# Optimization experiments

Hardware: AMD Instinct MI355X
Metric: run time of the kernel (lower is better)

Reference implementation:

```python
import jax, jax.numpy as jnp
import numpy as np

B, CIN, COUT, H, W = 16, 64, 64, 256, 256
MX, MY = 64, 64  # retained spectral modes (NxW, NyW)
NY_R = W // 2 + 1  # rfft length of last dim


def _dequant(q, scale, min_val):
    # matches torch: (q.float() + 127) * scale + min_val, q in [-127, 128]
    return (q.astype(jnp.float32) + 127.0) * scale + min_val


def setup_inputs() -> dict:
    key = jax.random.key(0)
    k0, k1, k2, k3 = jax.random.split(key, 4)
    x = jax.random.normal(k0, (B, CIN, H, W), dtype=jnp.float32)
    q_real = jax.random.randint(k1, (CIN, COUT, MX, MY), -127, 129, dtype=jnp.int32)
    q_imag = jax.random.randint(k2, (CIN, COUT, MX, MY), -127, 129, dtype=jnp.int32)
    q_bias = jax.random.randint(k3, (COUT,), -127, 129, dtype=jnp.int32)
    return {
        "x": x,
        "q_real": q_real,
        "q_imag": q_imag,
        "q_bias": q_bias,
        "scale_real": jnp.float32(2e-3),
        "min_real": jnp.float32(-0.25),
        "scale_imag": jnp.float32(2e-3),
        "min_imag": jnp.float32(-0.25),
        "b_scale": jnp.float32(1e-4),
        "b_min": jnp.float32(-0.0128),
    }


def reference(x, q_real, q_imag, q_bias, scale_real, min_real, scale_imag, min_imag, b_scale, b_min):
    # 1) rFFT over the last two (spatial) dims, norm='backward' (torch default)
    x_fft = jnp.fft.rfftn(x, axes=(-2, -1), norm="backward")  # [B, Cin, H, NY_R] complex

    # 2) inline dequantize the complex spectral weight
    w_real = _dequant(q_real, scale_real, min_real)
    w_imag = _dequant(q_imag, scale_imag, min_imag)
    Wc = jax.lax.complex(w_real, w_imag)  # [Cin, Cout, MX, MY]

    # 3) center slices as in the torch forward
    cx, nx = H // 2, MX // 2
    sx = slice(cx - nx, cx + (MX - nx))
    cy, ny = NY_R // 2, MY // 2
    sy = slice(cy - ny, cy + (MY - ny))

    # fused channel multiply-accumulate (replaces the nested python loop)
    out_slice = jnp.einsum("bixy,ioxy->boxy", x_fft[:, :, sx, sy], Wc)

    out_fft = jnp.zeros((B, COUT, H, NY_R), dtype=x_fft.dtype)
    out_fft = out_fft.at[:, :, sx, sy].set(out_slice)

    # 4) inverse rFFT back to spatial domain
    x_out = jnp.fft.irfftn(out_fft, s=(H, W), axes=(-2, -1), norm="backward")

    # 5) dequantized bias, broadcast over (1, Cout, 1, 1)
    bias = _dequant(q_bias, b_scale, b_min)
    return x_out + bias[None, :, None, None]
```

## Files before the change

kernel.cpp:

```cpp
#include <hip/hip_runtime.h>


#define HW    256
#define NCIN  64
#define NCOUT 64
#define NB    16
#define R0    96
#define C0    32

typedef __bf16 bf16x2 __attribute__((ext_vector_type(2)));
typedef __bf16 bf16x8 __attribute__((ext_vector_type(8)));
typedef float  f32x4  __attribute__((ext_vector_type(4)));

__device__ __forceinline__ unsigned short f2bf(float f) {
    __bf16 h = (__bf16)f;
    return __builtin_bit_cast(unsigned short, h);
}
__device__ __forceinline__ unsigned pk2(float a, float b) {
    bf16x2 v;
    v.x = (__bf16)a;
    v.y = (__bf16)b;
    return __builtin_bit_cast(unsigned, v);
}
__device__ __forceinline__ bf16x8 ld_frag_g(const unsigned short* p) {
    return __builtin_bit_cast(bf16x8, *(const uint4*)p);
}
__device__ __forceinline__ void gload_lds16(const unsigned short* g, unsigned short* l) {
    __builtin_amdgcn_global_load_lds(
        (const __attribute__((address_space(1))) unsigned int*)g,
        (__attribute__((address_space(3))) unsigned int*)l, 16, 0, 0);
}

__global__ void build_tables2(unsigned short* __restrict__ A1tab,
                              unsigned short* __restrict__ B2T) {
    int idx = blockIdx.x * 256 + threadIdx.x;
    int h = idx >> 7;
    int k = idx & 127;
    int kk = k & 63;
    const float TPO = 0.0245436926061702596754f;
    float s, c;
    int m1 = (((R0 + kk) * h) & 255);
    sincosf((float)m1 * TPO, &s, &c);
    A1tab[idx] = f2bf(k < 64 ? c : s);
    int m2 = (((C0 + kk) * h) & 255);
    sincosf((float)m2 * TPO, &s, &c);
    B2T[idx] = f2bf(k < 64 ? c : -s);
}

__global__ void build_fwd_tables(unsigned short* __restrict__ B1fT,
                                 unsigned short* __restrict__ A2f) {
    int idx = blockIdx.x * 256 + threadIdx.x;
    const float TPO = 0.0245436926061702596754f;
    float s, c;
    if (idx < 32768) {
        int cc = idx >> 8, w = idx & 255;
        int m = (((C0 + (cc & 63)) * w) & 255);
        sincosf((float)m * TPO, &s, &c);
        int sidx = (cc << 8) | (w ^ ((cc & 7) << 3));
        B1fT[sidx] = f2bf(cc < 64 ? c : -s);
    } else {
        int j = idx - 32768;
        int mr = j >> 9, k = j & 511;
        int m = (((R0 + (mr & 63)) * (k & 255)) & 255);
        sincosf((float)m * TPO, &s, &c);
        float v = (mr < 64) ? ((k < 256) ? c : s)
                            : ((k < 256) ? -s : c);
        A2f[j] = f2bf(v);
    }
}

__global__ __launch_bounds__(256, 2) void fwd_mfma(
        const float*          __restrict__ x,
        const unsigned short* __restrict__ B1fT,
        const unsigned short* __restrict__ A2f,
        float*                __restrict__ Xout) {
    __shared__ __align__(16) unsigned short smem[32768];
    int bi = blockIdx.x;
    const float* xim = x + (size_t)bi * 65536;
    int t = threadIdx.x, lane = t & 63, wv = t >> 6;
    int g = lane >> 4, lr = lane & 15;

    #pragma unroll
    for (int i = 0; i < 16; ++i)
        gload_lds16(B1fT + i * 2048 + t * 8, &smem[i * 2048 + wv * 512]);

    const float* xrow[4];
    #pragma unroll
    for (int mf = 0; mf < 4; ++mf)
        xrow[mf] = xim + (wv * 64 + mf * 16 + lr) * 256 + g * 8;
    float4 xv[2][4][2];
    #pragma unroll
    for (int mf = 0; mf < 4; ++mf) {
        xv[0][mf][0] = *(const float4*)(xrow[mf]);
        xv[0][mf][1] = *(const float4*)(xrow[mf] + 4);
    }
    __syncthreads();

    f32x4 acc[4][8];
    #pragma unroll
    for (int mf = 0; mf < 4; ++mf)
        #pragma unroll
        for (int nf = 0; nf < 8; ++nf) acc[mf][nf] = (f32x4)0.0f;

    #pragma unroll
    for (int ks = 0; ks < 8; ++ks) {
        const int cur = ks & 1;
        if (ks < 7) {
            #pragma unroll
            for (int mf = 0; mf < 4; ++mf) {
                xv[cur ^ 1][mf][0] = *(const float4*)(xrow[mf] + (ks + 1) * 32);
                xv[cur ^ 1][mf][1] = *(const float4*)(xrow[mf] + (ks + 1) * 32 + 4);
            }
        }
        int k0 = ks * 32 + g * 8;
        bf16x8 b[8];
        #pragma unroll
        for (int nf = 0; nf < 8; ++nf) {
            int n = nf * 16 + lr;
            b[nf] = __builtin_bit_cast(bf16x8,
                      *(const uint4*)&smem[n * 256 + (k0 ^ ((n & 7) << 3))]);
        }
        bf16x8 a[4];
        #pragma unroll
        for (int mf = 0; mf < 4; ++mf) {
            uint4 pk;
            pk.x = pk2(xv[cur][mf][0].x, xv[cur][mf][0].y);
            pk.y = pk2(xv[cur][mf][0].z, xv[cur][mf][0].w);
            pk.z = pk2(xv[cur][mf][1].x, xv[cur][mf][1].y);
            pk.w = pk2(xv[cur][mf][1].z, xv[cur][mf][1].w);
            a[mf] = __builtin_bit_cast(bf16x8, pk);
        }
        #pragma unroll
        for (int mf = 0; mf < 4; ++mf)
            #pragma unroll
            for (int nf = 0; nf < 8; ++nf)
                acc[mf][nf] = __builtin_amdgcn_mfma_f32_16x16x32_bf16(
                                  a[mf], b[nf], acc[mf][nf], 0, 0, 0);
    }
    __syncthreads();

    #pragma unroll
    for (int mf = 0; mf < 4; ++mf)
        #pragma unroll
        for (int nf = 0; nf < 8; ++nf) {
            int cl  = nf * 16 + lr;
            int col = cl & 63;
            int h0  = wv * 64 + mf * 16 + g * 4;
            int kk0 = (cl < 64) ? h0 : (256 + h0);
            uint2 pk;
            pk.x = pk2(acc[mf][nf][0], acc[mf][nf][1]);
            pk.y = pk2(acc[mf][nf][2], acc[mf][nf][3]);
            *(uint2*)&smem[col * 512 + (kk0 ^ ((col & 7) << 3))] = pk;
        }
    __syncthreads();

    f32x4 acc2[2][4];
    #pragma unroll
    for (int mf = 0; mf < 2; ++mf)
        #pragma unroll
        for (int nf = 0; nf < 4; ++nf) acc2[mf][nf] = (f32x4)0.0f;
    #pragma unroll
    for (int ks = 0; ks < 16; ++ks) {
        int k0 = ks * 32 + g * 8;
        bf16x8 a2[2], b2[4];
        #pragma unroll
        for (int mf = 0; mf < 2; ++mf) {
            int m = wv * 32 + mf * 16 + lr;
            a2[mf] = ld_frag_g(A2f + m * 512 + k0);
        }
        #pragma unroll
        for (int nf = 0; nf < 4; ++nf) {
            int c = nf * 16 + lr;
            b2[nf] = __builtin_bit_cast(bf16x8,
                       *(const uint4*)&smem[c * 512 + (k0 ^ ((c & 7) << 3))]);
        }
        #pragma unroll
        for (int mf = 0; mf < 2; ++mf)
            #pragma unroll
            for (int nf = 0; nf < 4; ++nf)
                acc2[mf][nf] = __builtin_amdgcn_mfma_f32_16x16x32_bf16(
                                   a2[mf], b2[nf], acc2[mf][nf], 0, 0, 0);
    }
    float* Xp = Xout + (size_t)bi * 8192;
    #pragma unroll
    for (int mf = 0; mf < 2; ++mf)
        #pragma unroll
        for (int nf = 0; nf < 4; ++nf)
            #pragma unroll
            for (int rg = 0; rg < 4; ++rg) {
                int m = wv * 32 + mf * 16 + g * 4 + rg;
                int c = nf * 16 + lr;
                Xp[(m >> 6) * 4096 + (m & 63) * 64 + c] = acc2[mf][nf][rg];
            }
}

__global__ __launch_bounds__(256) void mix_kernel(
        const float* __restrict__ X,
        const int*   __restrict__ q_real,
        const int*   __restrict__ q_imag,
        const float* __restrict__ s_r, const float* __restrict__ m_r,
        const float* __restrict__ s_i, const float* __restrict__ m_i,
        float2*      __restrict__ Y) {
    int rr = blockIdx.x;
    int ot = blockIdx.y;
    int t  = threadIdx.x;
    int cp = t & 31;
    int oq = t >> 5;
    int o  = ot * 8 + oq;
    int c0 = cp * 2;
    float sr = *s_r, mr = *m_r, si = *s_i, mi = *m_i;

    __shared__ float xr_sh[2][16][72];
    __shared__ float xi_sh[2][16][72];

    int sb  = t >> 4;
    int scq = t & 15;
    const float* xbase = X + (size_t)sb * 64 * 8192 + rr * 64 + scq * 4;

    const int* qrp = q_real + (size_t)o * 4096 + rr * 64 + c0;
    const int* qip = q_imag + (size_t)o * 4096 + rr * 64 + c0;

    float Yr0[16], Yi0[16], Yr1[16], Yi1[16];
    #pragma unroll
    for (int b = 0; b < 16; ++b) { Yr0[b] = 0.f; Yi0[b] = 0.f; Yr1[b] = 0.f; Yi1[b] = 0.f; }

    int2 wqr[2], wqi[2];
    wqr[0] = *(const int2*)(qrp);
    wqi[0] = *(const int2*)(qip);
    wqr[1] = *(const int2*)(qrp + 262144);
    wqi[1] = *(const int2*)(qip + 262144);
    {
        float4 gr = *(const float4*)(xbase);
        float4 gi = *(const float4*)(xbase + 4096);
        *(float4*)&xr_sh[0][sb][scq * 4] = gr;
        *(float4*)&xi_sh[0][sb][scq * 4] = gi;
    }
    __syncthreads();

    #pragma unroll 2
    for (int i = 0; i < 64; ++i) {
        const int cur = i & 1;
        float4 gr, gi;
        if (i < 63) {
            gr = *(const float4*)(xbase + (size_t)(i + 1) * 8192);
            gi = *(const float4*)(xbase + (size_t)(i + 1) * 8192 + 4096);
        }
        float wr0 = (float)(wqr[cur].x + 127) * sr + mr;
        float wr1 = (float)(wqr[cur].y + 127) * sr + mr;
        float wi0 = (float)(wqi[cur].x + 127) * si + mi;
        float wi1 = (float)(wqi[cur].y + 127) * si + mi;
        if (i < 62) {
            wqr[cur] = *(const int2*)(qrp + (size_t)(i + 2) * 262144);
            wqi[cur] = *(const int2*)(qip + (size_t)(i + 2) * 262144);
        }
        #pragma unroll
        for (int b = 0; b < 16; ++b) {
            float2 xr = *(const float2*)&xr_sh[cur][b][c0];
            float2 xi = *(const float2*)&xi_sh[cur][b][c0];
            Yr0[b] += xr.x * wr0 - xi.x * wi0;
            Yi0[b] += xr.x * wi0 + xi.x * wr0;
            Yr1[b] += xr.y * wr1 - xi.y * wi1;
            Yi1[b] += xr.y * wi1 + xi.y * wr1;
        }
        if (i < 63) {
            *(float4*)&xr_sh[cur ^ 1][sb][scq * 4] = gr;
            *(float4*)&xi_sh[cur ^ 1][sb][scq * 4] = gi;
            __syncthreads();
        }
    }

    #pragma unroll
    for (int b = 0; b < 16; ++b) {
        float4 v = make_float4(Yr0[b], Yi0[b], Yr1[b], Yi1[b]);
        *(float4*)&Y[(size_t)b * 262144 + (size_t)o * 4096 + rr * 64 + c0] = v;
    }
}

__global__ __launch_bounds__(256, 2) void inv_mfma(
        const float2*         __restrict__ Y,
        const unsigned short* __restrict__ A1tab,
        const unsigned short* __restrict__ B2T,
        const int*            __restrict__ q_bias,
        const float* __restrict__ b_s, const float* __restrict__ b_m,
        float*                __restrict__ out) {
    __shared__ __align__(16) unsigned short smem[32768];
    int bo   = blockIdx.x;
    int t    = threadIdx.x;
    int lane = t & 63;
    int wv   = t >> 6;
    int g    = lane >> 4;
    int lr   = lane & 15;
    float bias = ((float)q_bias[bo & 63] + 127.0f) * (*b_s) + (*b_m);

    const float2* Yp = Y + (size_t)bo * 4096;
    for (int l = t; l < 4096; l += 256) {
        int r = l >> 6, c = l & 63;
        float2 y = Yp[l];
        unsigned short yr  = f2bf(y.x);
        unsigned short yi  = f2bf(y.y);
        unsigned short nyi = f2bf(-y.y);
        int sw = (c & 7) << 3;
        smem[c * 128        + ((r)      ^ sw)] = yr;
        smem[c * 128        + ((64 + r) ^ sw)] = nyi;
        smem[(64 + c) * 128 + ((r)      ^ sw)] = yi;
        smem[(64 + c) * 128 + ((64 + r) ^ sw)] = yr;
    }
    __syncthreads();

    f32x4 acc[4][8];
    #pragma unroll
    for (int mf = 0; mf < 4; ++mf)
        #pragma unroll
        for (int nf = 0; nf < 8; ++nf) acc[mf][nf] = (f32x4)0.0f;

    #pragma unroll
    for (int ks = 0; ks < 4; ++ks) {
        int k0 = ks * 32 + g * 8;
        bf16x8 a[4], b[8];
        #pragma unroll
        for (int mf = 0; mf < 4; ++mf) {
            int h = wv * 64 + mf * 16 + lr;
            a[mf] = ld_frag_g(A1tab + h * 128 + k0);
        }
        #pragma unroll
        for (int nf = 0; nf < 8; ++nf) {
            int n = nf * 16 + lr;
            b[nf] = ld_frag_g(&smem[n * 128 + (k0 ^ ((n & 7) << 3))]);
        }
        #pragma unroll
        for (int mf = 0; mf < 4; ++mf)
            #pragma unroll
            for (int nf = 0; nf < 8; ++nf)
                acc[mf][nf] = __builtin_amdgcn_mfma_f32_16x16x32_bf16(
                                  a[mf], b[nf], acc[mf][nf], 0, 0, 0);
    }
    __syncthreads();

    #pragma unroll
    for (int mf = 0; mf < 4; ++mf)
        #pragma unroll
        for (int nf = 0; nf < 8; ++nf)
            #pragma unroll
            for (int rg = 0; rg < 4; ++rg) {
                int h = wv * 64 + mf * 16 + g * 4 + rg;
                int k = nf * 16 + lr;
                smem[h * 128 + (k ^ ((h & 7) << 3))] = f2bf(acc[mf][nf][rg]);
            }
    __syncthreads();

    const float scale = 2.0f / 65536.0f;
    float* outp = out + (size_t)bo * 65536;
    #pragma unroll
    for (int nh = 0; nh < 2; ++nh) {
        f32x4 acc2[4][8];
        #pragma unroll
        for (int mf = 0; mf < 4; ++mf)
            #pragma unroll
            for (int nf = 0; nf < 8; ++nf) acc2[mf][nf] = (f32x4)0.0f;

        #pragma unroll
        for (int ks = 0; ks < 4; ++ks) {
            int k0 = ks * 32 + g * 8;
            bf16x8 a[4], b[8];
            #pragma unroll
            for (int mf = 0; mf < 4; ++mf) {
                int h = wv * 64 + mf * 16 + lr;
                a[mf] = ld_frag_g(&smem[h * 128 + (k0 ^ ((h & 7) << 3))]);
            }
            #pragma unroll
            for (int nf = 0; nf < 8; ++nf) {
                int w = nh * 128 + nf * 16 + lr;
                b[nf] = ld_frag_g(B2T + w * 128 + k0);
            }
            #pragma unroll
            for (int mf = 0; mf < 4; ++mf)
                #pragma unroll
                for (int nf = 0; nf < 8; ++nf)
                    acc2[mf][nf] = __builtin_amdgcn_mfma_f32_16x16x32_bf16(
                                       a[mf], b[nf], acc2[mf][nf], 0, 0, 0);
        }
        #pragma unroll
        for (int mf = 0; mf < 4; ++mf)
            #pragma unroll
            for (int rg = 0; rg < 4; ++rg) {
                int h = wv * 64 + mf * 16 + g * 4 + rg;
                float* row = outp + h * 256 + nh * 128 + lr;
                #pragma unroll
                for (int nf = 0; nf < 8; ++nf)
                    row[nf * 16] = acc2[mf][nf][rg] * scale + bias;
            }
    }
}

extern "C" void kernel_launch(void* const* d_in, const int* in_sizes, int n_in,
                              void* d_out, int out_size, void* d_ws, size_t ws_size,
                              hipStream_t stream) {
    const float* x          = (const float*)d_in[0];
    const int*   q_real     = (const int*)  d_in[1];
    const int*   q_imag     = (const int*)  d_in[2];
    const int*   q_bias     = (const int*)  d_in[3];
    const float* scale_real = (const float*)d_in[4];
    const float* min_real   = (const float*)d_in[5];
    const float* scale_imag = (const float*)d_in[6];
    const float* min_imag   = (const float*)d_in[7];
    const float* b_scale    = (const float*)d_in[8];
    const float* b_min      = (const float*)d_in[9];
    float* out = (float*)d_out;

    float* ws = (float*)d_ws;
    unsigned short* A1tab = (unsigned short*)(ws);
    unsigned short* B2T   = (unsigned short*)(ws + 16384);
    unsigned short* B1fT  = (unsigned short*)(ws + 32768);
    unsigned short* A2f   = (unsigned short*)(ws + 49152);
    float*          Xws   = (float*) (ws + 81920);
    float2*         Yws   = (float2*)(ws + 81920 + 8388608);

    build_tables2<<<128, 256, 0, stream>>>(A1tab, B2T);
    build_fwd_tables<<<384, 256, 0, stream>>>(B1fT, A2f);
    fwd_mfma<<<NB * NCIN, 256, 0, stream>>>(x, B1fT, A2f, Xws);
    mix_kernel<<<dim3(64, 8), 256, 0, stream>>>(Xws, q_real, q_imag,
                                                scale_real, min_real,
                                                scale_imag, min_imag, Yws);
    inv_mfma<<<NB * NCOUT, 256, 0, stream>>>(Yws, A1tab, B2T,
                                             q_bias, b_scale, b_min, out);
}
```

Measured before the change: 279.9 us.

## Relayout spectral intermediate, use direct global-to-LDS loads, store mixed spectrum as bf16

The forward kernel now writes its spectrum in a row-major-by-mode layout, so each mix block reads one contiguous 2048-float slab per input channel. The mix kernel stages that slab with global_load_lds instead of loading through registers and then writing to shared memory. The mix output is packed to bf16 real/imag pairs, which halves the Y intermediate and lets the inverse kernel read it with wide vector loads and negate the imaginary part by flipping the sign bit. This cuts memory traffic and register staging between kernels, at the cost of rounding Y to bf16 earlier; the inverse kernel already converted it to bf16.

```diff
diff --git a/kernel.cpp b/kernel.cpp
--- a/kernel.cpp
+++ b/kernel.cpp
@@ -26,6 +26,11 @@
     return __builtin_bit_cast(bf16x8, *(const uint4*)p);
 }
 __device__ __forceinline__ void gload_lds16(const unsigned short* g, unsigned short* l) {
+    __builtin_amdgcn_global_load_lds(
+        (const __attribute__((address_space(1))) unsigned int*)g,
+        (__attribute__((address_space(3))) unsigned int*)l, 16, 0, 0);
+}
+__device__ __forceinline__ void gload_lds16f(const float* g, float* l) {
     __builtin_amdgcn_global_load_lds(
         (const __attribute__((address_space(1))) unsigned int*)g,
         (__attribute__((address_space(3))) unsigned int*)l, 16, 0, 0);
@@ -181,17 +186,21 @@
                 acc2[mf][nf] = __builtin_amdgcn_mfma_f32_16x16x32_bf16(
                                    a2[mf], b2[nf], acc2[mf][nf], 0, 0, 0);
     }
-    float* Xp = Xout + (size_t)bi * 8192;
-    #pragma unroll
-    for (int mf = 0; mf < 2; ++mf)
-        #pragma unroll
-        for (int nf = 0; nf < 4; ++nf)
-            #pragma unroll
-            for (int rg = 0; rg < 4; ++rg) {
-                int m = wv * 32 + mf * 16 + g * 4 + rg;
-                int c = nf * 16 + lr;
-                Xp[(m >> 6) * 4096 + (m & 63) * 64 + c] = acc2[mf][nf][rg];
-            }
+    {
+        int bb = bi >> 6, ii = bi & 63;
+        #pragma unroll
+        for (int mf = 0; mf < 2; ++mf)
+            #pragma unroll
+            for (int nf = 0; nf < 4; ++nf)
+                #pragma unroll
+                for (int rg = 0; rg < 4; ++rg) {
+                    int m = wv * 32 + mf * 16 + g * 4 + rg;
+                    int c = nf * 16 + lr;
+                    int r = m & 63, p = m >> 6;
+                    Xout[(size_t)r * 131072 + ii * 2048 + bb * 128 + p * 64 + c]
+                        = acc2[mf][nf][rg];
+                }
+    }
 }
 
 __global__ __launch_bounds__(256) void mix_kernel(
@@ -200,22 +209,18 @@
         const int*   __restrict__ q_imag,
         const float* __restrict__ s_r, const float* __restrict__ m_r,
         const float* __restrict__ s_i, const float* __restrict__ m_i,
-        float2*      __restrict__ Y) {
+        unsigned*    __restrict__ Yb) {
     int rr = blockIdx.x;
     int ot = blockIdx.y;
-    int t  = threadIdx.x;
+    int t  = threadIdx.x, lane = t & 63, wv = t >> 6;
     int cp = t & 31;
     int oq = t >> 5;
     int o  = ot * 8 + oq;
     int c0 = cp * 2;
     float sr = *s_r, mr = *m_r, si = *s_i, mi = *m_i;
 
-    __shared__ float xr_sh[2][16][72];
-    __shared__ float xi_sh[2][16][72];
-
-    int sb  = t >> 4;
-    int scq = t & 15;
-    const float* xbase = X + (size_t)sb * 64 * 8192 + rr * 64 + scq * 4;
+    __shared__ __align__(16) float sh[2][2048];
+    const float* xsl = X + (size_t)rr * 131072;
 
     const int* qrp = q_real + (size_t)o * 4096 + rr * 64 + c0;
     const int* qip = q_imag + (size_t)o * 4096 + rr * 64 + c0;
@@ -230,20 +235,19 @@
     wqr[1] = *(const int2*)(qrp + 262144);
     wqi[1] = *(const int2*)(qip + 262144);
     {
-        float4 gr = *(const float4*)(xbase);
-        float4 gi = *(const float4*)(xbase + 4096);
-        *(float4*)&xr_sh[0][sb][scq * 4] = gr;
-        *(float4*)&xi_sh[0][sb][scq * 4] = gi;
+        const float* src = xsl + wv * 512;
+        gload_lds16f(src + lane * 4,       &sh[0][wv * 512]);
+        gload_lds16f(src + 256 + lane * 4, &sh[0][wv * 512 + 256]);
     }
     __syncthreads();
 
     #pragma unroll 2
     for (int i = 0; i < 64; ++i) {
         const int cur = i & 1;
-        float4 gr, gi;
         if (i < 63) {
-            gr = *(const float4*)(xbase + (size_t)(i + 1) * 8192);
-            gi = *(const float4*)(xbase + (size_t)(i + 1) * 8192 + 4096);
+            const float* src = xsl + (i + 1) * 2048 + wv * 512;
+            gload_lds16f(src + lane * 4,       &sh[cur ^ 1][wv * 512]);
+            gload_lds16f(src + 256 + lane * 4, &sh[cur ^ 1][wv * 512 + 256]);
         }
         float wr0 = (float)(wqr[cur].x + 127) * sr + mr;
         float wr1 = (float)(wqr[cur].y + 127) * sr + mr;
@@ -255,29 +259,27 @@
         }
         #pragma unroll
         for (int b = 0; b < 16; ++b) {
-            float2 xr = *(const float2*)&xr_sh[cur][b][c0];
-            float2 xi = *(const float2*)&xi_sh[cur][b][c0];
+            float2 xr = *(const float2*)&sh[cur][b * 128 + c0];
+            float2 xi = *(const float2*)&sh[cur][b * 128 + 64 + c0];
             Yr0[b] += xr.x * wr0 - xi.x * wi0;
             Yi0[b] += xr.x * wi0 + xi.x * wr0;
             Yr1[b] += xr.y * wr1 - xi.y * wi1;
             Yi1[b] += xr.y * wi1 + xi.y * wr1;
         }
-        if (i < 63) {
-            *(float4*)&xr_sh[cur ^ 1][sb][scq * 4] = gr;
-            *(float4*)&xi_sh[cur ^ 1][sb][scq * 4] = gi;
-            __syncthreads();
-        }
+        if (i < 63) __syncthreads();
     }
 
     #pragma unroll
     for (int b = 0; b < 16; ++b) {
-        float4 v = make_float4(Yr0[b], Yi0[b], Yr1[b], Yi1[b]);
-        *(float4*)&Y[(size_t)b * 262144 + (size_t)o * 4096 + rr * 64 + c0] = v;
+        uint2 v;
+        v.x = pk2(Yr0[b], Yi0[b]);
+        v.y = pk2(Yr1[b], Yi1[b]);
+        *(uint2*)&Yb[(size_t)(b * NCOUT + o) * 4096 + rr * 64 + c0] = v;
     }
 }
 
 __global__ __launch_bounds__(256, 2) void inv_mfma(
-        const float2*         __restrict__ Y,
+        const unsigned*       __restrict__ Y,
         const unsigned short* __restrict__ A1tab,
         const unsigned short* __restrict__ B2T,
         const int*            __restrict__ q_bias,
@@ -292,18 +294,29 @@
     int lr   = lane & 15;
     float bias = ((float)q_bias[bo & 63] + 127.0f) * (*b_s) + (*b_m);
 
-    const float2* Yp = Y + (size_t)bo * 4096;
-    for (int l = t; l < 4096; l += 256) {
-        int r = l >> 6, c = l & 63;
-        float2 y = Yp[l];
-        unsigned short yr  = f2bf(y.x);
-        unsigned short yi  = f2bf(y.y);
-        unsigned short nyi = f2bf(-y.y);
-        int sw = (c & 7) << 3;
-        smem[c * 128        + ((r)      ^ sw)] = yr;
-        smem[c * 128        + ((64 + r) ^ sw)] = nyi;
-        smem[(64 + c) * 128 + ((r)      ^ sw)] = yi;
-        smem[(64 + c) * 128 + ((64 + r) ^ sw)] = yr;
+    {
+        const unsigned* Yp = Y + (size_t)bo * 4096;
+        uint4 y0 = *(const uint4*)(Yp + t * 16);
+        uint4 y1 = *(const uint4*)(Yp + t * 16 + 4);
+        uint4 y2 = *(const uint4*)(Yp + t * 16 + 8);
+        uint4 y3 = *(const uint4*)(Yp + t * 16 + 12);
+        unsigned ys[16] = {y0.x, y0.y, y0.z, y0.w, y1.x, y1.y, y1.z, y1.w,
+                           y2.x, y2.y, y2.z, y2.w, y3.x, y3.y, y3.z, y3.w};
+        int r  = t >> 2;
+        int cb = (t & 3) * 16;
+        #pragma unroll
+        for (int j = 0; j < 16; ++j) {
+            int c = cb + j;
+            unsigned y = ys[j];
+            unsigned short yr  = (unsigned short)(y & 0xFFFFu);
+            unsigned short yi  = (unsigned short)(y >> 16);
+            unsigned short nyi = (unsigned short)(yi ^ 0x8000u);
+            int sw = (c & 7) << 3;
+            smem[c * 128        + ((r)      ^ sw)] = yr;
+            smem[c * 128        + ((64 + r) ^ sw)] = nyi;
+            smem[(64 + c) * 128 + ((r)      ^ sw)] = yi;
+            smem[(64 + c) * 128 + ((64 + r) ^ sw)] = yr;
+        }
     }
     __syncthreads();
 
@@ -412,15 +425,15 @@
     unsigned short* B2T   = (unsigned short*)(ws + 16384);
     unsigned short* B1fT  = (unsigned short*)(ws + 32768);
     unsigned short* A2f   = (unsigned short*)(ws + 49152);
-    float*          Xws   = (float*) (ws + 81920);
-    float2*         Yws   = (float2*)(ws + 81920 + 8388608);
+    float*          Xws   = (float*)   (ws + 81920);
+    unsigned*       Ybws  = (unsigned*)(ws + 81920 + 8388608);
 
     build_tables2<<<128, 256, 0, stream>>>(A1tab, B2T);
     build_fwd_tables<<<384, 256, 0, stream>>>(B1fT, A2f);
     fwd_mfma<<<NB * NCIN, 256, 0, stream>>>(x, B1fT, A2f, Xws);
     mix_kernel<<<dim3(64, 8), 256, 0, stream>>>(Xws, q_real, q_imag,
                                                 scale_real, min_real,
-                                                scale_imag, min_imag, Yws);
-    inv_mfma<<<NB * NCOUT, 256, 0, stream>>>(Yws, A1tab, B2T,
+                                                scale_imag, min_imag, Ybws);
+    inv_mfma<<<NB * NCOUT, 256, 0, stream>>>(Ybws, A1tab, B2T,
                                              q_bias, b_scale, b_min, out);
 }
```

Measured after the change: 277.0 us. No clear change (-1.0%).
